# Optimization experiments

Measured on AMD Instinct MI355X. Metric: run time of the kernel, lower is better.

Reference implementation:

```python
import jax, jax.numpy as jnp
import numpy as np

B, S, D, H = 2, 2048, 2048, 16
HD = D // H  # head_dim = 128

def _rope_tables(head_dim, context_length, theta_base=10000.0):
    inv_freq = 1.0 / theta_base ** (jnp.arange(0, head_dim, 2, dtype=jnp.float32) / head_dim)
    pos = jnp.arange(context_length, dtype=jnp.float32)
    angles = pos[:, None] * inv_freq[None, :]            # [S, HD/2]
    angles = jnp.concatenate([angles, angles], axis=1)   # [S, HD]
    return jnp.cos(angles), jnp.sin(angles)

def _apply_rope(x, cos, sin):
    # x: [b, h, s, hd]; cos/sin: [s, hd]
    hd = x.shape[-1]
    x1, x2 = x[..., : hd // 2], x[..., hd // 2 :]
    rotated = jnp.concatenate([-x2, x1], axis=-1)
    return x * cos[None, None] + rotated * sin[None, None]

def setup_inputs() -> dict:
    key = jax.random.key(0)
    ks = jax.random.split(key, 5)
    x = jax.random.normal(ks[0], (B, S, D), dtype=jnp.float32)
    scale = 1.0 / np.sqrt(D)
    Wq = jax.random.normal(ks[1], (D, D), dtype=jnp.float32) * scale
    Wk = jax.random.normal(ks[2], (D, D), dtype=jnp.float32) * scale
    Wv = jax.random.normal(ks[3], (D, D), dtype=jnp.float32) * scale
    Wo = jax.random.normal(ks[4], (D, D), dtype=jnp.float32) * scale
    cos, sin = _rope_tables(HD, S)
    return {"x": x, "Wq": Wq, "Wk": Wk, "Wv": Wv, "Wo": Wo, "cos": cos, "sin": sin}

def reference(x, Wq, Wk, Wv, Wo, cos, sin):
    b, s, _ = x.shape
    def split_heads(t):  # [b,s,D] -> [b,H,s,HD]
        return t.reshape(b, s, H, HD).transpose(0, 2, 1, 3)
    q = split_heads(x @ Wq.T)
    k = split_heads(x @ Wk.T)
    v = split_heads(x @ Wv.T)
    q = _apply_rope(q, cos[:s], sin[:s])
    k = _apply_rope(k, cos[:s], sin[:s])
    scores = jnp.einsum("bhqd,bhkd->bhqk", q, k) / np.sqrt(HD)
    causal = jnp.triu(jnp.ones((s, s), dtype=bool), k=1)
    scores = jnp.where(causal[None, None], -jnp.inf, scores)
    weights = jax.nn.softmax(scores, axis=-1)
    ctx = jnp.einsum("bhqk,bhkd->bhqd", weights, v)
    ctx = ctx.transpose(0, 2, 1, 3).reshape(b, s, D)
    return ctx @ Wo.T
```

## Files before the change

### kernel.cpp

```cpp
#include <hip/hip_runtime.h>
#include <cstdint>
#include <cmath>

#define B_ 2
#define S_ 2048
#define D_ 2048
#define H_ 16
#define HD_ 128

#define NEG_SENTINEL -1.0e30f

typedef __bf16 bf16;
typedef __attribute__((ext_vector_type(4))) __bf16 bf16x4;
typedef __attribute__((ext_vector_type(8))) __bf16 bf16x8;
typedef __attribute__((ext_vector_type(4))) float f32x4;

__device__ __forceinline__ void gload_lds16(const void* g, void* l) {
  __builtin_amdgcn_global_load_lds(
      (const __attribute__((address_space(1))) unsigned int*)g,
      (__attribute__((address_space(3))) unsigned int*)l, 16, 0, 0);
}

__device__ __forceinline__ f32x4 mfma16(bf16x8 a, bf16x8 b, f32x4 c) {
  return __builtin_amdgcn_mfma_f32_16x16x32_bf16(a, b, c, 0, 0, 0);
}

__global__ __launch_bounds__(256) void cvt_f32_bf16(
    const float* __restrict__ in, bf16* __restrict__ out)
{
  int i = blockIdx.x * 256 + threadIdx.x;
  f32x4 v = ((const f32x4*)in)[i];
  bf16x4 o;
#pragma unroll
  for (int j = 0; j < 4; ++j) o[j] = (bf16)v[j];
  ((bf16x4*)out)[i] = o;
}

__global__ __launch_bounds__(256) void cvt_qkvx(
    const float* __restrict__ x, bf16* __restrict__ xb,
    const float* __restrict__ wq, const float* __restrict__ wk,
    const float* __restrict__ wv, bf16* __restrict__ wout)
{
  int b = (int)blockIdx.x;
  const float* in; bf16* out; int base;
  if (b < 8192)      { in = x;  out = xb; base = b; }
  else {
    int r = b - 8192; int j = r >> 12; base = r & 4095;
    if (j == 0)      { in = wq; out = wout; }
    else if (j == 1) { in = wk; out = wout + 4194304; }
    else             { in = wv; out = wout + 8388608; }
  }
  int i = base * 256 + threadIdx.x;
  f32x4 v = ((const f32x4*)in)[i];
  bf16x4 o;
#pragma unroll
  for (int t2 = 0; t2 < 4; ++t2) o[t2] = (bf16)v[t2];
  ((bf16x4*)out)[i] = o;
}

#define GTM 128
#define GTN 128
#define GBK 64

template <typename OT>
__global__ __launch_bounds__(256) void gemm_xwt(
    const bf16* __restrict__ A, const bf16* __restrict__ W, OT* __restrict__ C,
    int M, int N, int K, int ldc)
{
  __shared__ bf16 sA[GTM * GBK];
  __shared__ bf16 sB[GTN * GBK];
  const int tid  = threadIdx.x;
  const int wave = tid >> 6, lane = tid & 63;
  const int quad = lane >> 4, l16 = lane & 15;
  const int tm = blockIdx.y * GTM;
  const int tn = blockIdx.x * GTN;
  const int wm = (wave >> 1) * 64, wn = (wave & 1) * 64;

  f32x4 acc[4][4];
#pragma unroll
  for (int i = 0; i < 4; ++i)
#pragma unroll
    for (int j = 0; j < 4; ++j) acc[i][j] = (f32x4)0.0f;

  for (int k0 = 0; k0 < K; k0 += GBK) {
    __syncthreads();
#pragma unroll
    for (int g = 0; g < 4; ++g) {
      int gb  = (g * 4 + wave) * 64;
      int p   = gb + lane;
      int row = p >> 3, pos = p & 7;
      int cc  = pos ^ (row & 7);
      gload_lds16(A + (size_t)(tm + row) * K + k0 + cc * 8, (char*)sA + (size_t)gb * 16);
      gload_lds16(W + (size_t)(tn + row) * K + k0 + cc * 8, (char*)sB + (size_t)gb * 16);
    }
    __syncthreads();

#pragma unroll
    for (int t = 0; t < 2; ++t) {
      bf16x8 af[4], bfr[4];
#pragma unroll
      for (int i = 0; i < 4; ++i) {
        int rowa = wm + i * 16 + l16;
        int posa = (t * 4 + quad) ^ (rowa & 7);
        af[i] = *(const bf16x8*)(sA + rowa * GBK + posa * 8);
        int rowb = wn + i * 16 + l16;
        int posb = (t * 4 + quad) ^ (rowb & 7);
        bfr[i] = *(const bf16x8*)(sB + rowb * GBK + posb * 8);
      }
#pragma unroll
      for (int i = 0; i < 4; ++i)
#pragma unroll
        for (int j = 0; j < 4; ++j)
          acc[i][j] = mfma16(af[i], bfr[j], acc[i][j]);
    }
  }

#pragma unroll
  for (int i = 0; i < 4; ++i)
#pragma unroll
    for (int r = 0; r < 4; ++r) {
      int row = tm + wm + i * 16 + quad * 4 + r;
#pragma unroll
      for (int j = 0; j < 4; ++j) {
        int col = tn + wn + j * 16 + l16;
        C[(size_t)row * ldc + col] = (OT)acc[i][j][r];
      }
    }
}

__global__ __launch_bounds__(256) void rope_qk(
    bf16* __restrict__ Q, bf16* __restrict__ Kk,
    const float* __restrict__ cosT, const float* __restrict__ sinT, int rs)
{
  const float kappa = 0.08838834764831845f * 1.4426950408889634f;
  int t  = blockIdx.x * 256 + threadIdx.x;
  int d0 = (t & 7) * 8;
  int h  = (t >> 3) & (H_ - 1);
  int s  = (t >> 7) & (S_ - 1);
  int b  = t >> 18;
  size_t base = ((size_t)(b * S_ + s)) * rs + (size_t)h * HD_;

  const float* cl = cosT + s * HD_ + d0;
  const float* sl = sinT + s * HD_ + d0;

  bf16x8 ql = *(const bf16x8*)(Q + base + d0);
  bf16x8 qh = *(const bf16x8*)(Q + base + 64 + d0);
  bf16x8 kl = *(const bf16x8*)(Kk + base + d0);
  bf16x8 kh = *(const bf16x8*)(Kk + base + 64 + d0);

  bf16x8 qlo, qho, klo, kho;
#pragma unroll
  for (int i = 0; i < 8; ++i) {
    float c1 = cl[i], s1 = sl[i];
    float c2 = cl[64 + i], s2 = sl[64 + i];
    float x1 = (float)ql[i], x2 = (float)qh[i];
    qlo[i] = (bf16)((x1 * c1 - x2 * s1) * kappa);
    qho[i] = (bf16)((x2 * c2 + x1 * s2) * kappa);
    float y1 = (float)kl[i], y2 = (float)kh[i];
    klo[i] = (bf16)(y1 * c1 - y2 * s1);
    kho[i] = (bf16)(y2 * c2 + y1 * s2);
  }
  *(bf16x8*)(Q + base + d0)       = qlo;
  *(bf16x8*)(Q + base + 64 + d0)  = qho;
  *(bf16x8*)(Kk + base + d0)      = klo;
  *(bf16x8*)(Kk + base + 64 + d0) = kho;
}

__global__ __launch_bounds__(256) void transpose_v(
    const bf16* __restrict__ V, bf16* __restrict__ Vt, int rs)
{
  __shared__ bf16 sT[64 * 72];
  const int tid = threadIdx.x;
  const int si = blockIdx.x;
  const int di = blockIdx.y;
  const int bh = blockIdx.z;
  const int b  = bh >> 4, h = bh & 15;

  const bf16* src = V + (size_t)b * S_ * rs + (size_t)h * HD_ + di * 64;
  bf16*       dst = Vt + ((size_t)bh * HD_ + di * 64) * S_ + si * 64;

#pragma unroll
  for (int half = 0; half < 2; ++half) {
    int r  = half * 32 + (tid >> 3);
    int c0 = (tid & 7) * 8;
    bf16x8 v = *(const bf16x8*)(src + (size_t)(si * 64 + r) * rs + c0);
    *(bf16x8*)(sT + r * 72 + c0) = v;
  }
  __syncthreads();
#pragma unroll
  for (int half = 0; half < 2; ++half) {
    int dr = half * 32 + (tid >> 3);
    int c0 = (tid & 7) * 8;
    bf16x8 o;
#pragma unroll
    for (int j = 0; j < 8; ++j) o[j] = sT[(c0 + j) * 72 + dr];
    *(bf16x8*)(dst + (size_t)dr * S_ + c0) = o;
  }
}

#define ABK 64
#define SPS 72

__global__ __launch_bounds__(512) void attn_fwd(
    const bf16* __restrict__ Q, const bf16* __restrict__ K,
    const bf16* __restrict__ Vt, bf16* __restrict__ O, int rs)
{
  __shared__ bf16 sK[ABK * HD_];
  __shared__ bf16 sVT[HD_ * ABK];
  __shared__ bf16 sP[128 * SPS];

  const int tid  = threadIdx.x;
  const int wave = tid >> 6, lane = tid & 63;
  const int quad = lane >> 4, l16 = lane & 15;

  const int lin   = (int)blockIdx.x;
  const int low3  = lin & 7;
  const int rest  = lin >> 3;
  const int qt    = 15 - (rest & 15);
  const int colhi = rest >> 4;
  const int col   = low3 + (colhi << 3);
  const int b = col >> 4, h = col & 15;

  const bf16* Qh  = Q + (size_t)b * S_ * rs + (size_t)h * HD_;
  const bf16* Kh  = K + (size_t)b * S_ * rs + (size_t)h * HD_;
  const bf16* Vth = Vt + ((size_t)(b * H_ + h) * HD_) * S_;
  bf16*       Oh  = O + (size_t)b * S_ * D_ + (size_t)h * HD_;

  const int wq = wave * 16;
  const int q0 = qt * 128;
  const int wq_abs = q0 + wq;

  bf16x8 qf[4];
  {
    const bf16* rp = Qh + (size_t)(wq_abs + l16) * rs + quad * 8;
#pragma unroll
    for (int t = 0; t < 4; ++t) qf[t] = *(const bf16x8*)(rp + t * 32);
  }

  f32x4 o_acc[8];
#pragma unroll
  for (int j = 0; j < 8; ++j) o_acc[j] = (f32x4)0.0f;
  float m_col = NEG_SENTINEL;
  float l_col = 0.0f;

  const int nkt = 2 * qt + 2;
#pragma unroll 1
  for (int kt = 0; kt < nkt; ++kt) {
    const int kk0 = kt * ABK;
    __syncthreads();

#pragma unroll
    for (int g = 0; g < 2; ++g) {
      int p   = g * 512 + tid;
      int row = p >> 4, pos = p & 15;
      int cc  = pos ^ (row & 15);
      gload_lds16(Kh + (size_t)(kk0 + row) * rs + cc * 8, (char*)sK + (size_t)p * 16);
    }
#pragma unroll
    for (int g = 0; g < 2; ++g) {
      int p  = g * 512 + tid;
      int d  = p >> 3, pos = p & 7;
      int cc = pos ^ (d & 7);
      gload_lds16(Vth + (size_t)d * S_ + kk0 + cc * 8, (char*)sVT + (size_t)p * 16);
    }
    __syncthreads();

    if (kk0 <= wq_abs + 15) {
      f32x4 st[4];
#pragma unroll
      for (int jt = 0; jt < 4; ++jt) {
        bf16x8 kf[4];
#pragma unroll
        for (int t = 0; t < 4; ++t) {
          int pos = (t * 4 + quad) ^ l16;
          kf[t] = *(const bf16x8*)(sK + (jt * 16 + l16) * HD_ + pos * 8);
        }
        f32x4 a2 = (f32x4)0.0f;
#pragma unroll
        for (int t = 0; t < 4; ++t) a2 = mfma16(kf[t], qf[t], a2);
        st[jt] = a2;
      }

      if (kk0 + 63 > wq_abs) {
        int qcol = wq_abs + l16;
#pragma unroll
        for (int jt = 0; jt < 4; ++jt)
#pragma unroll
          for (int r = 0; r < 4; ++r) {
            int key = kk0 + jt * 16 + quad * 4 + r;
            if (key > qcol) st[jt][r] = NEG_SENTINEL;
          }
      }

      float mx = NEG_SENTINEL;
#pragma unroll
      for (int jt = 0; jt < 4; ++jt)
#pragma unroll
        for (int r = 0; r < 4; ++r) mx = fmaxf(mx, st[jt][r]);
      mx = fmaxf(mx, __shfl_xor(mx, 16, 64));
      mx = fmaxf(mx, __shfl_xor(mx, 32, 64));
      float m_new = fmaxf(m_col, mx);
      float alpha = exp2f(m_col - m_new);
      float ts = 0.0f;
#pragma unroll
      for (int jt = 0; jt < 4; ++jt) {
        bf16x4 pk;
#pragma unroll
        for (int r = 0; r < 4; ++r) {
          float p = exp2f(st[jt][r] - m_new);
          ts += p;
          pk[r] = (bf16)p;
        }
        *(bf16x4*)(sP + (wq + l16) * SPS + jt * 16 + quad * 4) = pk;
      }
      ts += __shfl_xor(ts, 16, 64);
      ts += __shfl_xor(ts, 32, 64);
      l_col = l_col * alpha + ts;
      m_col = m_new;
#pragma unroll
      for (int r = 0; r < 4; ++r) {
        float av = __shfl(alpha, quad * 4 + r, 64);
#pragma unroll
        for (int jd = 0; jd < 8; ++jd) o_acc[jd][r] *= av;
      }

#pragma unroll
      for (int ks = 0; ks < 2; ++ks) {
        bf16x8 pf = *(const bf16x8*)(sP + (wq + l16) * SPS + ks * 32 + quad * 8);
#pragma unroll
        for (int jd = 0; jd < 8; ++jd) {
          int pos = (ks * 4 + quad) ^ (l16 & 7);
          bf16x8 vf = *(const bf16x8*)(sVT + (jd * 16 + l16) * ABK + pos * 8);
          o_acc[jd] = mfma16(pf, vf, o_acc[jd]);
        }
      }
    }
  }

#pragma unroll
  for (int r = 0; r < 4; ++r) {
    float lv = __shfl(l_col, quad * 4 + r, 64);
    float inv_l = 1.0f / lv;
    int row = wq_abs + quad * 4 + r;
#pragma unroll
    for (int jd = 0; jd < 8; ++jd) {
      int colo = jd * 16 + l16;
      Oh[(size_t)row * D_ + colo] = (bf16)(o_acc[jd][r] * inv_l);
    }
  }
}

extern "C" void kernel_launch(void* const* d_in, const int* in_sizes, int n_in,
                              void* d_out, int out_size, void* d_ws, size_t ws_size,
                              hipStream_t stream) {
  const float* x    = (const float*)d_in[0];
  const float* Wq   = (const float*)d_in[1];
  const float* Wk   = (const float*)d_in[2];
  const float* Wv   = (const float*)d_in[3];
  const float* Wo   = (const float*)d_in[4];
  const float* cosT = (const float*)d_in[5];
  const float* sinT = (const float*)d_in[6];
  float* out = (float*)d_out;

  const size_t NE = (size_t)B_ * S_ * D_;
  const size_t WE = (size_t)D_ * D_;
  const int M = B_ * S_;
  const int cvtX = (int)(NE / 1024);
  const int cvtW = (int)(WE / 1024);
  const int ropeG = (B_ * S_ * H_ * 8) / 256;

  if (ws_size >= (size_t)92274688) {
    bf16* QKV   = (bf16*)d_ws;
    bf16* xb    = QKV + (size_t)M * 6144;
    bf16* Wqkv  = xb + NE;
    bf16* ctx   = Wqkv;
    bf16* Wob   = Wqkv + 2 * WE;
    bf16* Vt    = xb;

    cvt_qkvx<<<8192 + 3 * 4096, 256, 0, stream>>>(x, xb, Wq, Wk, Wv, Wqkv);
    gemm_xwt<bf16><<<dim3(48, 32), 256, 0, stream>>>(xb, Wqkv, QKV, M, 3 * D_, D_, 3 * D_);
    rope_qk<<<ropeG, 256, 0, stream>>>(QKV, QKV + D_, cosT, sinT, 3 * D_);
    transpose_v<<<dim3(32, 2, 32), 256, 0, stream>>>(QKV + 2 * D_, Vt, 3 * D_);
    attn_fwd<<<512, 512, 0, stream>>>(QKV, QKV + D_, Vt, ctx, 3 * D_);
    cvt_f32_bf16<<<cvtW, 256, 0, stream>>>(Wo, Wob);
    gemm_xwt<float><<<dim3(16, 32), 256, 0, stream>>>(ctx, Wob, out, M, D_, D_, D_);
  } else {
    bf16* Qb    = (bf16*)d_ws;
    bf16* Kb    = Qb + NE;
    bf16* Vb    = Kb + NE;
    bf16* Cb    = Vb + NE;
    bf16* Wslot = Cb + NE;

    cvt_f32_bf16<<<cvtX, 256, 0, stream>>>(x, Cb);
    cvt_f32_bf16<<<cvtW, 256, 0, stream>>>(Wq, Wslot);
    gemm_xwt<bf16><<<dim3(16, 32), 256, 0, stream>>>(Cb, Wslot, Qb, M, D_, D_, D_);
    cvt_f32_bf16<<<cvtW, 256, 0, stream>>>(Wk, Wslot);
    gemm_xwt<bf16><<<dim3(16, 32), 256, 0, stream>>>(Cb, Wslot, Kb, M, D_, D_, D_);
    cvt_f32_bf16<<<cvtW, 256, 0, stream>>>(Wv, Wslot);
    gemm_xwt<bf16><<<dim3(16, 32), 256, 0, stream>>>(Cb, Wslot, Vb, M, D_, D_, D_);
    rope_qk<<<ropeG, 256, 0, stream>>>(Qb, Kb, cosT, sinT, D_);
    transpose_v<<<dim3(32, 2, 32), 256, 0, stream>>>(Vb, Cb, D_);
    attn_fwd<<<512, 512, 0, stream>>>(Qb, Kb, Cb, Vb, D_);
    cvt_f32_bf16<<<cvtW, 256, 0, stream>>>(Wo, Wslot);
    gemm_xwt<float><<<dim3(16, 32), 256, 0, stream>>>(Vb, Wslot, out, M, D_, D_, D_);
  }
}
```

Baseline: 408.5 us.

## Double-buffer K/V tiles in attention and pair causal query tiles per block

The attention kernel now double-buffers K and V^T tiles in LDS, issuing the next tile's async global-to-LDS loads before computing on the current one. This replaces the two barriers per iteration with a single wait-and-barrier at the end. Each block now handles two query tiles (qt and 15-qt) in sequence, so every block gets the same causal workload, and the grid is halved to 256 blocks. LDS use doubles for K/V, which may lower occupancy, and having only 256 blocks may leave some compute units idle.

```diff
diff --git a/kernel.cpp b/kernel.cpp
--- a/kernel.cpp
+++ b/kernel.cpp
@@ -24,6 +24,14 @@
 __device__ __forceinline__ f32x4 mfma16(bf16x8 a, bf16x8 b, f32x4 c) {
   return __builtin_amdgcn_mfma_f32_16x16x32_bf16(a, b, c, 0, 0, 0);
 }
+
+__device__ __forceinline__ void wg_barrier() {
+  asm volatile("" ::: "memory");
+  __builtin_amdgcn_s_barrier();
+  asm volatile("" ::: "memory");
+}
+
+#define AVM0() asm volatile("s_waitcnt vmcnt(0)" ::: "memory")
 
 __global__ __launch_bounds__(256) void cvt_f32_bf16(
     const float* __restrict__ in, bf16* __restrict__ out)
@@ -201,12 +209,34 @@
 #define ABK 64
 #define SPS 72
 
+#define AK_STAGE(kt_, b_) do { \
+    int kk_ = (kt_) * ABK; \
+    _Pragma("unroll") \
+    for (int g_ = 0; g_ < 2; ++g_) { \
+      int p_   = g_ * 512 + tid; \
+      int row_ = p_ >> 4, pos_ = p_ & 15; \
+      int cc_  = pos_ ^ (row_ & 15); \
+      gload_lds16(Kh + (size_t)(kk_ + row_) * rs + cc_ * 8, \
+                  (char*)sK + (b_) * 16384 + (size_t)p_ * 16); \
+    } } while (0)
+
+#define AV_STAGE(kt_, b_) do { \
+    int kk_ = (kt_) * ABK; \
+    _Pragma("unroll") \
+    for (int g_ = 0; g_ < 2; ++g_) { \
+      int p_  = g_ * 512 + tid; \
+      int d_  = p_ >> 3, pos_ = p_ & 7; \
+      int cc_ = pos_ ^ (d_ & 7); \
+      gload_lds16(Vth + (size_t)d_ * S_ + kk_ + cc_ * 8, \
+                  (char*)sVT + (b_) * 16384 + (size_t)p_ * 16); \
+    } } while (0)
+
 __global__ __launch_bounds__(512) void attn_fwd(
     const bf16* __restrict__ Q, const bf16* __restrict__ K,
     const bf16* __restrict__ Vt, bf16* __restrict__ O, int rs)
 {
-  __shared__ bf16 sK[ABK * HD_];
-  __shared__ bf16 sVT[HD_ * ABK];
+  __shared__ bf16 sK[2 * ABK * HD_];
+  __shared__ bf16 sVT[2 * HD_ * ABK];
   __shared__ bf16 sP[128 * SPS];
 
   const int tid  = threadIdx.x;
@@ -216,8 +246,8 @@
   const int lin   = (int)blockIdx.x;
   const int low3  = lin & 7;
   const int rest  = lin >> 3;
-  const int qt    = 15 - (rest & 15);
-  const int colhi = rest >> 4;
+  const int pairx = rest & 7;
+  const int colhi = rest >> 3;
   const int col   = low3 + (colhi << 3);
   const int b = col >> 4, h = col & 15;
 
@@ -227,125 +257,131 @@
   bf16*       Oh  = O + (size_t)b * S_ * D_ + (size_t)h * HD_;
 
   const int wq = wave * 16;
-  const int q0 = qt * 128;
-  const int wq_abs = q0 + wq;
-
-  bf16x8 qf[4];
-  {
-    const bf16* rp = Qh + (size_t)(wq_abs + l16) * rs + quad * 8;
-#pragma unroll
-    for (int t = 0; t < 4; ++t) qf[t] = *(const bf16x8*)(rp + t * 32);
-  }
-
-  f32x4 o_acc[8];
-#pragma unroll
-  for (int j = 0; j < 8; ++j) o_acc[j] = (f32x4)0.0f;
-  float m_col = NEG_SENTINEL;
-  float l_col = 0.0f;
-
-  const int nkt = 2 * qt + 2;
+
 #pragma unroll 1
-  for (int kt = 0; kt < nkt; ++kt) {
-    const int kk0 = kt * ABK;
-    __syncthreads();
-
-#pragma unroll
-    for (int g = 0; g < 2; ++g) {
-      int p   = g * 512 + tid;
-      int row = p >> 4, pos = p & 15;
-      int cc  = pos ^ (row & 15);
-      gload_lds16(Kh + (size_t)(kk0 + row) * rs + cc * 8, (char*)sK + (size_t)p * 16);
-    }
-#pragma unroll
-    for (int g = 0; g < 2; ++g) {
-      int p  = g * 512 + tid;
-      int d  = p >> 3, pos = p & 7;
-      int cc = pos ^ (d & 7);
-      gload_lds16(Vth + (size_t)d * S_ + kk0 + cc * 8, (char*)sVT + (size_t)p * 16);
-    }
-    __syncthreads();
-
-    if (kk0 <= wq_abs + 15) {
-      f32x4 st[4];
-#pragma unroll
-      for (int jt = 0; jt < 4; ++jt) {
-        bf16x8 kf[4];
-#pragma unroll
-        for (int t = 0; t < 4; ++t) {
-          int pos = (t * 4 + quad) ^ l16;
-          kf[t] = *(const bf16x8*)(sK + (jt * 16 + l16) * HD_ + pos * 8);
+  for (int seg = 0; seg < 2; ++seg) {
+    const int qt = seg == 0 ? pairx : 15 - pairx;
+    const int q0 = qt * 128;
+    const int wq_abs = q0 + wq;
+
+    bf16x8 qf[4];
+    {
+      const bf16* rp = Qh + (size_t)(wq_abs + l16) * rs + quad * 8;
+#pragma unroll
+      for (int t = 0; t < 4; ++t) qf[t] = *(const bf16x8*)(rp + t * 32);
+    }
+
+    f32x4 o_acc[8];
+#pragma unroll
+    for (int j = 0; j < 8; ++j) o_acc[j] = (f32x4)0.0f;
+    float m_col = NEG_SENTINEL;
+    float l_col = 0.0f;
+
+    const int nkt = 2 * qt + 2;
+
+    AK_STAGE(0, 0);
+    AV_STAGE(0, 0);
+    AVM0();
+    wg_barrier();
+
+    int cur = 0;
+#pragma unroll 1
+    for (int kt = 0; kt < nkt; ++kt) {
+      const int kk0 = kt * ABK;
+      const bf16* sKc = sK + cur * (ABK * HD_);
+      const bf16* sVc = sVT + cur * (HD_ * ABK);
+
+      if (kt + 1 < nkt) {
+        AK_STAGE(kt + 1, cur ^ 1);
+        AV_STAGE(kt + 1, cur ^ 1);
+      }
+
+      if (kk0 <= wq_abs + 15) {
+        f32x4 st[4];
+#pragma unroll
+        for (int jt = 0; jt < 4; ++jt) {
+          bf16x8 kf[4];
+#pragma unroll
+          for (int t = 0; t < 4; ++t) {
+            int pos = (t * 4 + quad) ^ l16;
+            kf[t] = *(const bf16x8*)(sKc + (jt * 16 + l16) * HD_ + pos * 8);
+          }
+          f32x4 a2 = (f32x4)0.0f;
+#pragma unroll
+          for (int t = 0; t < 4; ++t) a2 = mfma16(kf[t], qf[t], a2);
+          st[jt] = a2;
         }
-        f32x4 a2 = (f32x4)0.0f;
-#pragma unroll
-        for (int t = 0; t < 4; ++t) a2 = mfma16(kf[t], qf[t], a2);
-        st[jt] = a2;
-      }
-
-      if (kk0 + 63 > wq_abs) {
-        int qcol = wq_abs + l16;
+
+        if (kk0 + 63 > wq_abs) {
+          int qcol = wq_abs + l16;
+#pragma unroll
+          for (int jt = 0; jt < 4; ++jt)
+#pragma unroll
+            for (int r = 0; r < 4; ++r) {
+              int key = kk0 + jt * 16 + quad * 4 + r;
+              if (key > qcol) st[jt][r] = NEG_SENTINEL;
+            }
+        }
+
+        float mx = NEG_SENTINEL;
 #pragma unroll
         for (int jt = 0; jt < 4; ++jt)
 #pragma unroll
+          for (int r = 0; r < 4; ++r) mx = fmaxf(mx, st[jt][r]);
+        mx = fmaxf(mx, __shfl_xor(mx, 16, 64));
+        mx = fmaxf(mx, __shfl_xor(mx, 32, 64));
+        float m_new = fmaxf(m_col, mx);
+        float alpha = exp2f(m_col - m_new);
+        float ts = 0.0f;
+#pragma unroll
+        for (int jt = 0; jt < 4; ++jt) {
+          bf16x4 pk;
+#pragma unroll
           for (int r = 0; r < 4; ++r) {
-            int key = kk0 + jt * 16 + quad * 4 + r;
-            if (key > qcol) st[jt][r] = NEG_SENTINEL;
+            float p = exp2f(st[jt][r] - m_new);
+            ts += p;
+            pk[r] = (bf16)p;
           }
-      }
-
-      float mx = NEG_SENTINEL;
-#pragma unroll
-      for (int jt = 0; jt < 4; ++jt)
-#pragma unroll
-        for (int r = 0; r < 4; ++r) mx = fmaxf(mx, st[jt][r]);
-      mx = fmaxf(mx, __shfl_xor(mx, 16, 64));
-      mx = fmaxf(mx, __shfl_xor(mx, 32, 64));
-      float m_new = fmaxf(m_col, mx);
-      float alpha = exp2f(m_col - m_new);
-      float ts = 0.0f;
-#pragma unroll
-      for (int jt = 0; jt < 4; ++jt) {
-        bf16x4 pk;
+          *(bf16x4*)(sP + (wq + l16) * SPS + jt * 16 + quad * 4) = pk;
+        }
+        ts += __shfl_xor(ts, 16, 64);
+        ts += __shfl_xor(ts, 32, 64);
+        l_col = l_col * alpha + ts;
+        m_col = m_new;
 #pragma unroll
         for (int r = 0; r < 4; ++r) {
-          float p = exp2f(st[jt][r] - m_new);
-          ts += p;
-          pk[r] = (bf16)p;
+          float av = __shfl(alpha, quad * 4 + r, 64);
+#pragma unroll
+          for (int jd = 0; jd < 8; ++jd) o_acc[jd][r] *= av;
         }
-        *(bf16x4*)(sP + (wq + l16) * SPS + jt * 16 + quad * 4) = pk;
-      }
-      ts += __shfl_xor(ts, 16, 64);
-      ts += __shfl_xor(ts, 32, 64);
-      l_col = l_col * alpha + ts;
-      m_col = m_new;
-#pragma unroll
-      for (int r = 0; r < 4; ++r) {
-        float av = __shfl(alpha, quad * 4 + r, 64);
-#pragma unroll
-        for (int jd = 0; jd < 8; ++jd) o_acc[jd][r] *= av;
-      }
-
-#pragma unroll
-      for (int ks = 0; ks < 2; ++ks) {
-        bf16x8 pf = *(const bf16x8*)(sP + (wq + l16) * SPS + ks * 32 + quad * 8);
-#pragma unroll
-        for (int jd = 0; jd < 8; ++jd) {
-          int pos = (ks * 4 + quad) ^ (l16 & 7);
-          bf16x8 vf = *(const bf16x8*)(sVT + (jd * 16 + l16) * ABK + pos * 8);
-          o_acc[jd] = mfma16(pf, vf, o_acc[jd]);
+
+#pragma unroll
+        for (int ks = 0; ks < 2; ++ks) {
+          bf16x8 pf = *(const bf16x8*)(sP + (wq + l16) * SPS + ks * 32 + quad * 8);
+#pragma unroll
+          for (int jd = 0; jd < 8; ++jd) {
+            int pos = (ks * 4 + quad) ^ (l16 & 7);
+            bf16x8 vf = *(const bf16x8*)(sVc + (jd * 16 + l16) * ABK + pos * 8);
+            o_acc[jd] = mfma16(pf, vf, o_acc[jd]);
+          }
         }
       }
-    }
-  }
-
-#pragma unroll
-  for (int r = 0; r < 4; ++r) {
-    float lv = __shfl(l_col, quad * 4 + r, 64);
-    float inv_l = 1.0f / lv;
-    int row = wq_abs + quad * 4 + r;
-#pragma unroll
-    for (int jd = 0; jd < 8; ++jd) {
-      int colo = jd * 16 + l16;
-      Oh[(size_t)row * D_ + colo] = (bf16)(o_acc[jd][r] * inv_l);
+
+      AVM0();
+      wg_barrier();
+      cur ^= 1;
+    }
+
+#pragma unroll
+    for (int r = 0; r < 4; ++r) {
+      float lv = __shfl(l_col, quad * 4 + r, 64);
+      float inv_l = 1.0f / lv;
+      int row = wq_abs + quad * 4 + r;
+#pragma unroll
+      for (int jd = 0; jd < 8; ++jd) {
+        int colo = jd * 16 + l16;
+        Oh[(size_t)row * D_ + colo] = (bf16)(o_acc[jd][r] * inv_l);
+      }
     }
   }
 }
@@ -381,7 +417,7 @@
     gemm_xwt<bf16><<<dim3(48, 32), 256, 0, stream>>>(xb, Wqkv, QKV, M, 3 * D_, D_, 3 * D_);
     rope_qk<<<ropeG, 256, 0, stream>>>(QKV, QKV + D_, cosT, sinT, 3 * D_);
     transpose_v<<<dim3(32, 2, 32), 256, 0, stream>>>(QKV + 2 * D_, Vt, 3 * D_);
-    attn_fwd<<<512, 512, 0, stream>>>(QKV, QKV + D_, Vt, ctx, 3 * D_);
+    attn_fwd<<<256, 512, 0, stream>>>(QKV, QKV + D_, Vt, ctx, 3 * D_);
     cvt_f32_bf16<<<cvtW, 256, 0, stream>>>(Wo, Wob);
     gemm_xwt<float><<<dim3(16, 32), 256, 0, stream>>>(ctx, Wob, out, M, D_, D_, D_);
   } else {
@@ -400,7 +436,7 @@
     gemm_xwt<bf16><<<dim3(16, 32), 256, 0, stream>>>(Cb, Wslot, Vb, M, D_, D_, D_);
     rope_qk<<<ropeG, 256, 0, stream>>>(Qb, Kb, cosT, sinT, D_);
     transpose_v<<<dim3(32, 2, 32), 256, 0, stream>>>(Vb, Cb, D_);
-    attn_fwd<<<512, 512, 0, stream>>>(Qb, Kb, Cb, Vb, D_);
+    attn_fwd<<<256, 512, 0, stream>>>(Qb, Kb, Cb, Vb, D_);
     cvt_f32_bf16<<<cvtW, 256, 0, stream>>>(Wo, Wslot);
     gemm_xwt<float><<<dim3(16, 32), 256, 0, stream>>>(Vb, Wslot, out, M, D_, D_, D_);
   }
```

New measurement: 379.8 us. 7.0% less time.
